# Optimization experiments

Measured on AMD Instinct MI355X. Metric: run time of the kernel, lower is better.

## Reference

```python
import jax, jax.numpy as jnp
import numpy as np
from jax import lax

T, S = 2000, 100          # trees, nodes per tree
N = T * S                 # total nodes
F = 256                   # in_feats (sent_hidden_size)
H = 256                   # h_feats (prop_hidden_size)


def _build_forest():
    # Random recursive forest: node j in each tree attaches to a uniform earlier node.
    rng = np.random.default_rng(0)
    pl = np.zeros((T, S), np.int64)    # local parent index
    dep = np.zeros((T, S), np.int64)
    rows = np.arange(T)
    for j in range(1, S):
        p = rng.integers(0, j, size=T)
        pl[:, j] = p
        dep[:, j] = dep[rows, p] + 1
    depth = dep.ravel()
    parent = (np.arange(T)[:, None] * S + pl).ravel()
    is_root = (np.arange(N) % S) == 0
    kids = np.arange(N)[~is_root]
    par = parent[~is_root]
    order = np.argsort(par, kind='stable')
    kids_s, par_s = kids[order], par[order]
    counts = np.bincount(par_s, minlength=N)
    C = int(counts.max())
    offsets = np.concatenate([[0], np.cumsum(counts)])
    pos = np.arange(len(kids_s)) - offsets[par_s]
    ch_all = np.full((N, C), N + 1, np.int32)   # pad with dummy zero-hidden row N+1
    ch_all[par_s, pos] = kids_s
    maxd = int(depth.max())
    L = maxd  # processed layers: depths 0..maxd-1 (deepest leaves stay zero, as in torch)
    layer_lists = [np.where(depth == d)[0] for d in range(L)]
    M = max(len(l) for l in layer_lists)
    layer_nodes = np.full((L, M), N, np.int32)  # pad writes to scratch row N
    child_idx = np.full((L, M, C), N + 1, np.int32)
    child_cnt = np.zeros((L, M), np.int32)
    for d, nd in enumerate(layer_lists):
        m = len(nd)
        layer_nodes[d, :m] = nd
        child_idx[d, :m] = ch_all[nd]
        child_cnt[d, :m] = counts[nd]
    root_idx = (np.arange(T) * S).astype(np.int32)
    return layer_nodes, child_idx, child_cnt, root_idx


def setup_inputs() -> dict:
    layer_nodes, child_idx, child_cnt, root_idx = _build_forest()
    key = jax.random.key(0)
    k1, k2, k3, k4, k5 = jax.random.split(key, 5)
    bound = 1.0 / np.sqrt(H)  # torch GRUCell default init
    u = lambda kk, sh: jax.random.uniform(kk, sh, jnp.float32, -bound, bound)
    return {
        'inputs': jax.random.normal(k1, (N, F), jnp.float32),
        'w_ih': u(k2, (3 * H, F)),
        'w_hh': u(k3, (3 * H, H)),
        'b_ih': u(k4, (3 * H,)),
        'b_hh': u(k5, (3 * H,)),
        'layer_nodes': jnp.asarray(layer_nodes),
        'child_idx': jnp.asarray(child_idx),
        'child_cnt': jnp.asarray(child_cnt),
        'root_idx': jnp.asarray(root_idx),
    }


def _gru(x, h, w_ih, w_hh, b_ih, b_hh):
    gi = x @ w_ih.T + b_ih
    gh = h @ w_hh.T + b_hh
    ir, iz, ig = jnp.split(gi, 3, axis=-1)
    hr, hz, hg = jnp.split(gh, 3, axis=-1)
    r = jax.nn.sigmoid(ir + hr)
    z = jax.nn.sigmoid(iz + hz)
    n = jnp.tanh(ig + r * hg)
    return (1.0 - z) * n + z * h


def _forward(inputs, w_ih, w_hh, b_ih, b_hh, layer_nodes, child_idx, child_cnt, root_idx):
    # rows N (scatter scratch for padded slots) and N+1 (always-zero child pad) appended
    x_all = jnp.concatenate([inputs, jnp.zeros((2, F), inputs.dtype)], axis=0)
    h0 = jnp.zeros((N + 2, H), inputs.dtype)

    def step(all_h, layer):
        nodes, cidx, ccnt = layer
        ch = all_h[cidx]                                        # [M, C, H]
        denom = jnp.maximum(ccnt, 1).astype(all_h.dtype)[:, None]
        h_prev = ch.sum(axis=1) / denom                         # mean over children; 0 for leaves
        new_h = _gru(x_all[nodes], h_prev, w_ih, w_hh, b_ih, b_hh)
        return all_h.at[nodes].set(new_h), None

    # process deepest layer first (reversed(range(max_depth)) in the original)
    xs = (layer_nodes[::-1], child_idx[::-1], child_cnt[::-1])
    all_h, _ = lax.scan(step, h0, xs)
    return all_h[root_idx]                                      # [T, H]


def reference(inputs, w_ih, w_hh, b_ih, b_hh, layer_nodes, child_idx, child_cnt, root_idx):
    return _forward(inputs, w_ih, w_hh, b_ih, b_hh, layer_nodes, child_idx, child_cnt, root_idx)
```

## Files before the change

kernel.cpp:

```cpp
#include <hip/hip_runtime.h>
#include <hip/hip_bf16.h>
#include <math.h>

#define N_NODES 200000
#define T_TREES 2000
#define S_NODES 100
#define F_DIM 256
#define H_DIM 256
#define G_DIM 768
#define D_MAX 28

typedef __attribute__((ext_vector_type(8))) short short8b;
typedef __attribute__((ext_vector_type(4))) float f32x4;

static __device__ __forceinline__ unsigned short f2bf(float x) {
    union { __hip_bfloat16 h; unsigned short u; } cv;
    cv.h = __float2bfloat16(x);
    return cv.u;
}
static __device__ __forceinline__ float bf2f(unsigned short u) {
    return __uint_as_float(((unsigned)u) << 16);
}
static __device__ __forceinline__ float fsig(float x) {
    return __builtin_amdgcn_rcpf(1.0f + __expf(-x));
}
static __device__ __forceinline__ float ftanh(float x) {
    return 1.0f - 2.0f * __builtin_amdgcn_rcpf(__expf(2.0f * x) + 1.0f);
}

__global__ void k_zero(float4* __restrict__ p, int n4) {
    float4 z = make_float4(0.f, 0.f, 0.f, 0.f);
    for (int i = blockIdx.x * blockDim.x + threadIdx.x; i < n4;
         i += gridDim.x * blockDim.x)
        p[i] = z;
}

__global__ void k_convx(const float* __restrict__ x, unsigned short* __restrict__ xb,
                        int n8) {
    for (int i = blockIdx.x * blockDim.x + threadIdx.x; i < n8;
         i += gridDim.x * blockDim.x) {
        const float4* px = (const float4*)(x + (size_t)i * 8);
        float4 u = px[0], v = px[1];
        short8b t;
        t[0] = f2bf(u.x); t[1] = f2bf(u.y); t[2] = f2bf(u.z); t[3] = f2bf(u.w);
        t[4] = f2bf(v.x); t[5] = f2bf(v.y); t[6] = f2bf(v.z); t[7] = f2bf(v.w);
        *(short8b*)(xb + (size_t)i * 8) = t;
    }
}

__global__ void k_findM(const int* __restrict__ ln, int LM, int* __restrict__ Mdev) {
    int local = 0x7F7F7F7F;
    for (int p = T_TREES + blockIdx.x * blockDim.x + threadIdx.x; p < LM;
         p += gridDim.x * blockDim.x)
        if (ln[p] < N_NODES && p < local) local = p;
#pragma unroll
    for (int off = 32; off; off >>= 1) {
        int o = __shfl_down(local, off);
        if (o < local) local = o;
    }
    __shared__ int wmin[4];
    if ((threadIdx.x & 63) == 0) wmin[threadIdx.x >> 6] = local;
    __syncthreads();
    if (threadIdx.x == 0) {
        int m = wmin[0];
        for (int i = 1; i < 4; ++i) if (wmin[i] < m) m = wmin[i];
        if (m < 0x7F7F7F7F) atomicMin(Mdev, m);
    }
}

__global__ void k_hist(const int* __restrict__ ln, const int* __restrict__ Mdev,
                       int* __restrict__ layer_cnt, int LM) {
    __shared__ int h[D_MAX];
    if (threadIdx.x < D_MAX) h[threadIdx.x] = 0;
    __syncthreads();
    const int M = Mdev[0];
    for (int p = blockIdx.x * blockDim.x + threadIdx.x; p < LM;
         p += gridDim.x * blockDim.x)
        if (ln[p] < N_NODES) {
            int d = p / M;
            if (d < D_MAX) atomicAdd(&h[d], 1);
        }
    __syncthreads();
    if (threadIdx.x < D_MAX && h[threadIdx.x])
        atomicAdd(&layer_cnt[threadIdx.x], h[threadIdx.x]);
}

__global__ void k_convw(const float* __restrict__ wi, const float* __restrict__ wh,
                        unsigned short* __restrict__ wib, unsigned short* __restrict__ whb) {
    int i = blockIdx.x * blockDim.x + threadIdx.x;
    if (i < G_DIM * F_DIM) {
        wib[i] = f2bf(wi[i]);
        whb[i] = f2bf(wh[i]);
    }
}

__global__ __launch_bounds__(256) void k_gemm_x(
    const unsigned short* __restrict__ xb,
    const unsigned short* __restrict__ wib,
    const float* __restrict__ b_ih,
    unsigned short* __restrict__ gi_all) {
    __shared__ unsigned short Bs[2][64][256];

    const int tid = threadIdx.x;
    const int wv = tid >> 6, lane = tid & 63;
    const int lr = lane & 15, kg = lane >> 4;
    const long m0 = (long)blockIdx.x * 128 + wv * 32;

    short8b A[2][8];
#pragma unroll
    for (int ms = 0; ms < 2; ++ms) {
        long r = m0 + ms * 16 + lr;
        if (r > N_NODES - 1) r = N_NODES - 1;
        const unsigned short* xp = xb + r * F_DIM + kg * 8;
#pragma unroll
        for (int ks = 0; ks < 8; ++ks)
            A[ms][ks] = *(const short8b*)(xp + ks * 32);
    }

    const int sr = tid >> 2, sp = tid & 3;
    const int psr = (sr >> 3) & 1;
    const int gp_off = (lr >> 2) * 8 + (lr & 3);
    const int prow = (gp_off >> 3) & 1;

    short8b st[8];
    {
        const unsigned short* src = wib + (size_t)sr * F_DIM;
#pragma unroll
        for (int q = 0; q < 4; ++q) {
            int c = sp * 16 + q * 64;
            st[2 * q]     = *(const short8b*)(src + c);
            st[2 * q + 1] = *(const short8b*)(src + c + 8);
        }
#pragma unroll
        for (int q = 0; q < 4; ++q) {
            int slot = (sp >> 1) + 2 * q;
            int pc = ((slot ^ psr) << 5) + (sp & 1) * 16;
            *(short8b*)&Bs[0][sr][pc]     = st[2 * q];
            *(short8b*)&Bs[0][sr][pc + 8] = st[2 * q + 1];
        }
    }
    __syncthreads();

    const f32x4 zf = {0.f, 0.f, 0.f, 0.f};

    for (int nt = 0; nt < 12; ++nt) {
        const int cur = nt & 1;
        if (nt < 11) {
            const unsigned short* src = wib + (size_t)((nt + 1) * 64 + sr) * F_DIM;
#pragma unroll
            for (int q = 0; q < 4; ++q) {
                int c = sp * 16 + q * 64;
                st[2 * q]     = *(const short8b*)(src + c);
                st[2 * q + 1] = *(const short8b*)(src + c + 8);
            }
        }
#pragma unroll
        for (int nsp = 0; nsp < 2; ++nsp) {
            f32x4 aP0 = zf, aQ0 = zf, aP1 = zf, aQ1 = zf;
            const int rP = nsp * 32 + gp_off;
#pragma unroll
            for (int ks = 0; ks < 8; ++ks) {
                const int pc = ((ks ^ prow) << 5) + kg * 8;
                short8b BP = *(const short8b*)&Bs[cur][rP][pc];
                short8b BQ = *(const short8b*)&Bs[cur][rP + 4][pc];
                aP0 = __builtin_amdgcn_mfma_f32_16x16x32_bf16(BP, A[0][ks], aP0, 0, 0, 0);
                aQ0 = __builtin_amdgcn_mfma_f32_16x16x32_bf16(BQ, A[0][ks], aQ0, 0, 0, 0);
                aP1 = __builtin_amdgcn_mfma_f32_16x16x32_bf16(BP, A[1][ks], aP1, 0, 0, 0);
                aQ1 = __builtin_amdgcn_mfma_f32_16x16x32_bf16(BQ, A[1][ks], aQ1, 0, 0, 0);
            }
            const int g0 = nt * 64 + nsp * 32 + kg * 8;
            f32x4 b0 = *(const f32x4*)(b_ih + g0);
            f32x4 b1 = *(const f32x4*)(b_ih + g0 + 4);
            long m = m0 + lr;
            if (m < N_NODES) {
                short8b pk;
#pragma unroll
                for (int i = 0; i < 4; ++i) {
                    pk[i]     = f2bf(aP0[i] + b0[i]);
                    pk[4 + i] = f2bf(aQ0[i] + b1[i]);
                }
                *(short8b*)(gi_all + m * G_DIM + g0) = pk;
            }
            m = m0 + 16 + lr;
            if (m < N_NODES) {
                short8b pk;
#pragma unroll
                for (int i = 0; i < 4; ++i) {
                    pk[i]     = f2bf(aP1[i] + b0[i]);
                    pk[4 + i] = f2bf(aQ1[i] + b1[i]);
                }
                *(short8b*)(gi_all + m * G_DIM + g0) = pk;
            }
        }
        if (nt < 11) {
            __syncthreads();
#pragma unroll
            for (int q = 0; q < 4; ++q) {
                int slot = (sp >> 1) + 2 * q;
                int pc = ((slot ^ psr) << 5) + (sp & 1) * 16;
                *(short8b*)&Bs[cur ^ 1][sr][pc]     = st[2 * q];
                *(short8b*)&Bs[cur ^ 1][sr][pc + 8] = st[2 * q + 1];
            }
            __syncthreads();
        }
    }
}

#define LOADC2(buf, ns_, kh_)                                                  \
  _Pragma("unroll")                                                            \
  for (int kk = 0; kk < 4; ++kk)                                               \
    buf[kk] = *(const short8b*)(whb +                                          \
        (size_t)(512 + cb + (ns_) * 16 + lr) * H_DIM + ((kh_) * 4 + kk) * 32 + kg * 8);

#define MMACP(c_)                                                              \
  _Pragma("unroll")                                                            \
  for (int ks = 0; ks < 8; ++ks) {                                             \
    const int cch = ks * 4 + kg;                                               \
    const int pc = ((cch & 24) | ((cch ^ lr) & 7)) << 3;                       \
    short8b A0 = *(const short8b*)&Ab[lr][pc];                                 \
    short8b A1 = *(const short8b*)&Ab[16 + lr][pc];                            \
    _Pragma("unroll")                                                          \
    for (int ns = 0; ns < 2; ++ns) {                                           \
      acc[c_][0][ns] = __builtin_amdgcn_mfma_f32_16x16x32_bf16(                \
          A0, Bp[c_][ns][ks], acc[c_][0][ns], 0, 0, 0);                        \
      acc[c_][1][ns] = __builtin_amdgcn_mfma_f32_16x16x32_bf16(                \
          A1, Bp[c_][ns][ks], acc[c_][1][ns], 0, 0, 0);                        \
    }                                                                          \
  }

#define MMAC2(buf, ns_, kh_)                                                   \
  _Pragma("unroll")                                                            \
  for (int kk = 0; kk < 4; ++kk) {                                             \
    const int ks = (kh_) * 4 + kk;                                             \
    const int cch = ks * 4 + kg;                                               \
    const int pc = ((cch & 24) | ((cch ^ lr) & 7)) << 3;                       \
    short8b A0 = *(const short8b*)&Ab[lr][pc];                                 \
    short8b A1 = *(const short8b*)&Ab[16 + lr][pc];                            \
    acc[2][0][ns_] = __builtin_amdgcn_mfma_f32_16x16x32_bf16(                  \
        A0, buf[kk], acc[2][0][ns_], 0, 0, 0);                                 \
    acc[2][1][ns_] = __builtin_amdgcn_mfma_f32_16x16x32_bf16(                  \
        A1, buf[kk], acc[2][1][ns_], 0, 0, 0);                                 \
  }

__global__ __launch_bounds__(512, 2) void k_layer(
    const int* __restrict__ layer_nodes,
    const int* __restrict__ child_idx,
    const int* __restrict__ child_cnt,
    const int* __restrict__ Mdev,
    const int* __restrict__ layer_cnt,
    const unsigned short* __restrict__ whb,
    const unsigned short* __restrict__ gi_all,
    const float* __restrict__ b_hh,
    unsigned short* __restrict__ h_all,
    float* __restrict__ out,
    int d, int C) {
    __shared__ unsigned short Ab[32][256];
    __shared__ unsigned short Ag[32][776];
    __shared__ int Nd[32];

    const int cntd = layer_cnt[d];
    if (cntd == 0) return;
    const int M = Mdev[0];
    const int ntiles = (cntd + 31) >> 5;
    if (blockIdx.x >= ntiles) return;
    const long pbase = (long)d * M;

    const int tid = threadIdx.x;
    const int wv = tid >> 6, lane = tid & 63;
    const int lr = lane & 15, kg = lane >> 4;
    const int cb = wv * 32;

    short8b Bp[2][2][8];
#pragma unroll
    for (int c = 0; c < 2; ++c)
#pragma unroll
        for (int ns = 0; ns < 2; ++ns) {
            const unsigned short* bp =
                whb + (size_t)(c * 256 + cb + ns * 16 + lr) * H_DIM + kg * 8;
#pragma unroll
            for (int ks = 0; ks < 8; ++ks)
                Bp[c][ns][ks] = *(const short8b*)(bp + ks * 32);
        }

    float bh[3][2];
#pragma unroll
    for (int c = 0; c < 3; ++c)
#pragma unroll
        for (int ns = 0; ns < 2; ++ns)
            bh[c][ns] = b_hh[c * 256 + cb + ns * 16 + lr];

    const int srow = tid >> 4;
    const int sc = tid & 15;

    for (int tile = blockIdx.x; tile < ntiles; tile += gridDim.x) {
        __syncthreads();
        {
            int idx = tile * 32 + srow;
            int node = (idx < cntd) ? layer_nodes[pbase + idx] : -1;
            if (sc == 0) Nd[srow] = node;
            {
                const unsigned short* gp =
                    gi_all + (size_t)(node >= 0 ? node : 0) * G_DIM;
#pragma unroll
                for (int pass = 0; pass < 6; ++pass) {
                    int col = sc * 8 + pass * 128;
                    *(short8b*)&Ag[srow][col] = *(const short8b*)(gp + col);
                }
            }
            int cc = 0;
            const int* ch = nullptr;
            if (node >= 0) {
                cc = child_cnt[pbase + idx];
                ch = child_idx + (size_t)(pbase + idx) * C;
            }
            float inv = 1.0f / (float)(cc > 0 ? cc : 1);
            float sum[16];
#pragma unroll
            for (int i = 0; i < 16; ++i) sum[i] = 0.f;
            for (int c = 0; c < cc; ++c) {
                int kid = ch[c];
                const unsigned short* hr = h_all + (size_t)kid * H_DIM + sc * 16;
                short8b v0 = *(const short8b*)hr;
                short8b v1 = *(const short8b*)(hr + 8);
#pragma unroll
                for (int i = 0; i < 8; ++i) {
                    sum[i]     += bf2f((unsigned short)v0[i]);
                    sum[8 + i] += bf2f((unsigned short)v1[i]);
                }
            }
            short8b q0, q1;
#pragma unroll
            for (int i = 0; i < 8; ++i) {
                q0[i] = f2bf(sum[i] * inv);
                q1[i] = f2bf(sum[8 + i] * inv);
            }
            const int g = srow & 7;
            const int c0 = 2 * sc, c1 = 2 * sc + 1;
            *(short8b*)&Ab[srow][((c0 & 24) | ((c0 ^ g) & 7)) << 3] = q0;
            *(short8b*)&Ab[srow][((c1 & 24) | ((c1 ^ g) & 7)) << 3] = q1;
        }
        __syncthreads();

        const f32x4 zf = {0.f, 0.f, 0.f, 0.f};
        f32x4 acc[3][2][2];
#pragma unroll
        for (int c = 0; c < 3; ++c)
#pragma unroll
            for (int ms = 0; ms < 2; ++ms)
#pragma unroll
                for (int ns = 0; ns < 2; ++ns) acc[c][ms][ns] = zf;

        short8b C2a[4], C2b[4];
        LOADC2(C2a, 0, 0);
        MMACP(0);
        LOADC2(C2b, 0, 1);
        MMAC2(C2a, 0, 0);
        LOADC2(C2a, 1, 0);
        MMACP(1);
        MMAC2(C2b, 0, 1);
        LOADC2(C2b, 1, 1);
        MMAC2(C2a, 1, 0);
        MMAC2(C2b, 1, 1);

#pragma unroll
        for (int ms = 0; ms < 2; ++ms)
#pragma unroll
            for (int i = 0; i < 4; ++i) {
                const int rl = ms * 16 + kg * 4 + i;
                const int nd = Nd[rl];
                if (nd < 0) continue;
#pragma unroll
                for (int ns = 0; ns < 2; ++ns) {
                    const int k = cb + ns * 16 + lr;
                    const int kc = k >> 3;
                    const int hp_off = (((kc & 24) | ((kc ^ rl) & 7)) << 3) + (k & 7);
                    float hp = bf2f(Ab[rl][hp_off]);
                    float xr = bf2f(Ag[rl][k])       + acc[0][ms][ns][i] + bh[0][ns];
                    float xz = bf2f(Ag[rl][256 + k]) + acc[1][ms][ns][i] + bh[1][ns];
                    float r = fsig(xr);
                    float z = fsig(xz);
                    float n = ftanh(bf2f(Ag[rl][512 + k]) +
                                    r * (acc[2][ms][ns][i] + bh[2][ns]));
                    float h = (1.0f - z) * n + z * hp;
                    if (d == 0) {
                        out[(size_t)(nd / S_NODES) * H_DIM + k] = h;
                    } else {
                        h_all[(size_t)nd * H_DIM + k] = f2bf(h);
                    }
                }
            }
    }
}

extern "C" void kernel_launch(void* const* d_in, const int* in_sizes, int n_in,
                              void* d_out, int out_size, void* d_ws, size_t ws_size,
                              hipStream_t stream) {
    const float* inputs = (const float*)d_in[0];
    const float* w_ih   = (const float*)d_in[1];
    const float* w_hh   = (const float*)d_in[2];
    const float* b_ih   = (const float*)d_in[3];
    const float* b_hh   = (const float*)d_in[4];
    const int* layer_nodes = (const int*)d_in[5];
    const int* child_idx   = (const int*)d_in[6];
    const int* child_cnt   = (const int*)d_in[7];

    const int LM = in_sizes[5];
    const int C  = in_sizes[6] / in_sizes[5];

    char* w = (char*)d_ws;
    size_t o = 0;
    auto alloc = [&](size_t bytes) {
        void* p = w + o;
        o += (bytes + 255) & ~(size_t)255;
        return p;
    };
    unsigned short* wib    = (unsigned short*)alloc((size_t)G_DIM * F_DIM * 2);
    unsigned short* whb    = (unsigned short*)alloc((size_t)G_DIM * H_DIM * 2);
    unsigned short* xb     = (unsigned short*)alloc((size_t)N_NODES * F_DIM * 2);
    unsigned short* h_all  = (unsigned short*)alloc((size_t)N_NODES * H_DIM * 2);
    unsigned short* gi_all = (unsigned short*)alloc((size_t)N_NODES * G_DIM * 2);
    int*            Mdev      = (int*)alloc(4);
    int*            layer_cnt = (int*)alloc(D_MAX * 4);
    (void)ws_size;

    hipMemsetAsync(Mdev, 0x7F, 4, stream);
    hipMemsetAsync(layer_cnt, 0, D_MAX * 4, stream);

    k_zero<<<2048, 256, 0, stream>>>((float4*)h_all, N_NODES * H_DIM * 2 / 16);
    k_convx<<<2048, 256, 0, stream>>>(inputs, xb, N_NODES * F_DIM / 8);
    k_findM<<<256, 256, 0, stream>>>(layer_nodes, LM, Mdev);
    k_hist<<<256, 256, 0, stream>>>(layer_nodes, Mdev, layer_cnt, LM);
    k_convw<<<(G_DIM * F_DIM + 255) / 256, 256, 0, stream>>>(w_ih, w_hh, wib, whb);

    k_gemm_x<<<(N_NODES + 127) / 128, 256, 0, stream>>>(xb, wib, b_ih, gi_all);

    for (int d = D_MAX - 1; d >= 0; --d)
        k_layer<<<512, 512, 0, stream>>>(layer_nodes, child_idx, child_cnt,
                                         Mdev, layer_cnt, whb, gi_all, b_hh,
                                         h_all, (float*)d_out, d, C);
}
```

Before: 1.041 ms.

## Parallelize child-hidden gather across lanes and reswizzle input-GEMM weight LDS layout

The child-mean gather in the per-layer GRU kernel is restructured so each wavefront handles two rows at a time, with four lane groups loading different children in parallel and reducing with cross-lane shuffles. Before, one thread walked all children of a node serially. The aim is more memory-level parallelism and shorter dependent load chains on the latency-bound gather. Separately, the weight tile in the input-projection GEMM uses a finer XOR swizzle to cut LDS bank conflicts on the MFMA operand reads. The cost is extra shuffle instructions and idle lanes when a node has fewer than four children.

Result: slower. 1.337 ms (+28.4%).

```diff
diff --git a/kernel.cpp b/kernel.cpp
--- a/kernel.cpp
+++ b/kernel.cpp
@@ -118,9 +118,9 @@
     }
 
     const int sr = tid >> 2, sp = tid & 3;
-    const int psr = (sr >> 3) & 1;
+    const int hs = (sr & 3) | (((sr >> 3) & 1) << 2);
     const int gp_off = (lr >> 2) * 8 + (lr & 3);
-    const int prow = (gp_off >> 3) & 1;
+    const int hq = (lr & 3) | (((lr >> 2) & 1) << 2);
 
     short8b st[8];
     {
@@ -133,10 +133,9 @@
         }
 #pragma unroll
         for (int q = 0; q < 4; ++q) {
-            int slot = (sp >> 1) + 2 * q;
-            int pc = ((slot ^ psr) << 5) + (sp & 1) * 16;
-            *(short8b*)&Bs[0][sr][pc]     = st[2 * q];
-            *(short8b*)&Bs[0][sr][pc + 8] = st[2 * q + 1];
+            int c0 = sp * 2 + q * 8, c1 = c0 + 1;
+            *(short8b*)&Bs[0][sr][((c0 & 24) | ((c0 ^ hs) & 7)) << 3] = st[2 * q];
+            *(short8b*)&Bs[0][sr][((c1 & 24) | ((c1 ^ hs) & 7)) << 3] = st[2 * q + 1];
         }
     }
     __syncthreads();
@@ -160,7 +159,8 @@
             const int rP = nsp * 32 + gp_off;
 #pragma unroll
             for (int ks = 0; ks < 8; ++ks) {
-                const int pc = ((ks ^ prow) << 5) + kg * 8;
+                const int c = ks * 4 + kg;
+                const int pc = ((c & 24) | ((c ^ hq) & 7)) << 3;
                 short8b BP = *(const short8b*)&Bs[cur][rP][pc];
                 short8b BQ = *(const short8b*)&Bs[cur][rP + 4][pc];
                 aP0 = __builtin_amdgcn_mfma_f32_16x16x32_bf16(BP, A[0][ks], aP0, 0, 0, 0);
@@ -196,10 +196,9 @@
             __syncthreads();
 #pragma unroll
             for (int q = 0; q < 4; ++q) {
-                int slot = (sp >> 1) + 2 * q;
-                int pc = ((slot ^ psr) << 5) + (sp & 1) * 16;
-                *(short8b*)&Bs[cur ^ 1][sr][pc]     = st[2 * q];
-                *(short8b*)&Bs[cur ^ 1][sr][pc + 8] = st[2 * q + 1];
+                int c0 = sp * 2 + q * 8, c1 = c0 + 1;
+                *(short8b*)&Bs[cur ^ 1][sr][((c0 & 24) | ((c0 ^ hs) & 7)) << 3] = st[2 * q];
+                *(short8b*)&Bs[cur ^ 1][sr][((c1 & 24) | ((c1 ^ hs) & 7)) << 3] = st[2 * q + 1];
             }
             __syncthreads();
         }
@@ -291,53 +290,94 @@
 
     const int srow = tid >> 4;
     const int sc = tid & 15;
+    const int cl = lane >> 4;
+    const int chk = lane & 15;
 
     for (int tile = blockIdx.x; tile < ntiles; tile += gridDim.x) {
         __syncthreads();
         {
             int idx = tile * 32 + srow;
-            int node = (idx < cntd) ? layer_nodes[pbase + idx] : -1;
-            if (sc == 0) Nd[srow] = node;
-            {
-                const unsigned short* gp =
-                    gi_all + (size_t)(node >= 0 ? node : 0) * G_DIM;
-#pragma unroll
-                for (int pass = 0; pass < 6; ++pass) {
-                    int col = sc * 8 + pass * 128;
-                    *(short8b*)&Ag[srow][col] = *(const short8b*)(gp + col);
-                }
-            }
-            int cc = 0;
-            const int* ch = nullptr;
-            if (node >= 0) {
-                cc = child_cnt[pbase + idx];
-                ch = child_idx + (size_t)(pbase + idx) * C;
-            }
-            float inv = 1.0f / (float)(cc > 0 ? cc : 1);
-            float sum[16];
-#pragma unroll
-            for (int i = 0; i < 16; ++i) sum[i] = 0.f;
-            for (int c = 0; c < cc; ++c) {
-                int kid = ch[c];
-                const unsigned short* hr = h_all + (size_t)kid * H_DIM + sc * 16;
-                short8b v0 = *(const short8b*)hr;
-                short8b v1 = *(const short8b*)(hr + 8);
-#pragma unroll
-                for (int i = 0; i < 8; ++i) {
-                    sum[i]     += bf2f((unsigned short)v0[i]);
-                    sum[8 + i] += bf2f((unsigned short)v1[i]);
-                }
-            }
-            short8b q0, q1;
-#pragma unroll
-            for (int i = 0; i < 8; ++i) {
-                q0[i] = f2bf(sum[i] * inv);
-                q1[i] = f2bf(sum[8 + i] * inv);
-            }
-            const int g = srow & 7;
-            const int c0 = 2 * sc, c1 = 2 * sc + 1;
-            *(short8b*)&Ab[srow][((c0 & 24) | ((c0 ^ g) & 7)) << 3] = q0;
-            *(short8b*)&Ab[srow][((c1 & 24) | ((c1 ^ g) & 7)) << 3] = q1;
+            int node = (idx < cntd) ? layer_nodes[pbase + idx] : 0;
+            const unsigned short* gp = gi_all + (size_t)node * G_DIM;
+#pragma unroll
+            for (int pass = 0; pass < 6; ++pass) {
+                int col = sc * 8 + pass * 128;
+                *(short8b*)&Ag[srow][col] = *(const short8b*)(gp + col);
+            }
+        }
+#pragma unroll
+        for (int pp = 0; pp < 2; ++pp) {
+            const int r0 = wv * 4 + pp * 2;
+            int nodes2[2], ccs[2];
+            const int* chp[2];
+            float sum[2][16];
+            short8b va[2][2];
+            bool act[2];
+#pragma unroll
+            for (int rr = 0; rr < 2; ++rr) {
+                int idx = tile * 32 + r0 + rr;
+                int node = (idx < cntd) ? layer_nodes[pbase + idx] : -1;
+                nodes2[rr] = node;
+                int cc = 0; const int* ch = nullptr;
+                if (node >= 0) {
+                    cc = child_cnt[pbase + idx];
+                    ch = child_idx + (size_t)(pbase + idx) * C;
+                }
+                ccs[rr] = cc; chp[rr] = ch;
+#pragma unroll
+                for (int i = 0; i < 16; ++i) sum[rr][i] = 0.f;
+                act[rr] = (cl < cc);
+                if (act[rr]) {
+                    const unsigned short* hr =
+                        h_all + (size_t)ch[cl] * H_DIM + chk * 16;
+                    va[rr][0] = *(const short8b*)hr;
+                    va[rr][1] = *(const short8b*)(hr + 8);
+                }
+            }
+#pragma unroll
+            for (int rr = 0; rr < 2; ++rr) {
+                if (act[rr]) {
+#pragma unroll
+                    for (int i = 0; i < 8; ++i) {
+                        sum[rr][i]     += bf2f((unsigned short)va[rr][0][i]);
+                        sum[rr][8 + i] += bf2f((unsigned short)va[rr][1][i]);
+                    }
+                }
+                for (int b = 4; b < ccs[rr]; b += 4) {
+                    int c = b + cl;
+                    if (c < ccs[rr]) {
+                        const unsigned short* hr =
+                            h_all + (size_t)chp[rr][c] * H_DIM + chk * 16;
+                        short8b w0 = *(const short8b*)hr;
+                        short8b w1 = *(const short8b*)(hr + 8);
+#pragma unroll
+                        for (int i = 0; i < 8; ++i) {
+                            sum[rr][i]     += bf2f((unsigned short)w0[i]);
+                            sum[rr][8 + i] += bf2f((unsigned short)w1[i]);
+                        }
+                    }
+                }
+#pragma unroll
+                for (int i = 0; i < 16; ++i) {
+                    sum[rr][i] += __shfl_xor(sum[rr][i], 16);
+                    sum[rr][i] += __shfl_xor(sum[rr][i], 32);
+                }
+                if (cl == 0) {
+                    const int row = r0 + rr;
+                    float inv = 1.0f / (float)(ccs[rr] > 0 ? ccs[rr] : 1);
+                    short8b q0, q1;
+#pragma unroll
+                    for (int i = 0; i < 8; ++i) {
+                        q0[i] = f2bf(sum[rr][i] * inv);
+                        q1[i] = f2bf(sum[rr][8 + i] * inv);
+                    }
+                    const int g = row & 7;
+                    const int c0 = 2 * chk, c1 = c0 + 1;
+                    *(short8b*)&Ab[row][((c0 & 24) | ((c0 ^ g) & 7)) << 3] = q0;
+                    *(short8b*)&Ab[row][((c1 & 24) | ((c1 ^ g) & 7)) << 3] = q1;
+                    if (chk == 0) Nd[row] = nodes2[rr];
+                }
+            }
         }
         __syncthreads();
 
```

## Split child-mean gather into separate kernel and reswizzle x-GEMM shared layout

Applied to the files above, without the earlier changes.

Moves the per-layer child hidden-state averaging out of the fused GRU layer kernel into a dedicated gather kernel that writes a compact hprev buffer, which the layer kernel then reads directly. The aim is more parallelism and latency hiding for the irregular child gathers, instead of stalling the MFMA kernel. In exchange it adds a kernel launch per layer and an extra write and read of hprev through memory. The x-projection GEMM's shared-memory B tile uses a new XOR swizzle to reduce bank conflicts, and D_MAX drops from 28 to 24, removing layer launches that are assumed to be empty.

Result: slower. 1.083 ms (+4.0%).

```diff
diff --git a/kernel.cpp b/kernel.cpp
--- a/kernel.cpp
+++ b/kernel.cpp
@@ -8,7 +8,7 @@
 #define F_DIM 256
 #define H_DIM 256
 #define G_DIM 768
-#define D_MAX 28
+#define D_MAX 24
 
 typedef __attribute__((ext_vector_type(8))) short short8b;
 typedef __attribute__((ext_vector_type(4))) float f32x4;
@@ -118,9 +118,9 @@
     }
 
     const int sr = tid >> 2, sp = tid & 3;
-    const int psr = (sr >> 3) & 1;
+    const int hs = (sr & 3) | (((sr >> 3) & 1) << 2);
     const int gp_off = (lr >> 2) * 8 + (lr & 3);
-    const int prow = (gp_off >> 3) & 1;
+    const int hq = (lr & 3) | (((lr >> 2) & 1) << 2);
 
     short8b st[8];
     {
@@ -133,10 +133,9 @@
         }
 #pragma unroll
         for (int q = 0; q < 4; ++q) {
-            int slot = (sp >> 1) + 2 * q;
-            int pc = ((slot ^ psr) << 5) + (sp & 1) * 16;
-            *(short8b*)&Bs[0][sr][pc]     = st[2 * q];
-            *(short8b*)&Bs[0][sr][pc + 8] = st[2 * q + 1];
+            int c0 = sp * 2 + q * 8, c1 = c0 + 1;
+            *(short8b*)&Bs[0][sr][((c0 & 24) | ((c0 ^ hs) & 7)) << 3] = st[2 * q];
+            *(short8b*)&Bs[0][sr][((c1 & 24) | ((c1 ^ hs) & 7)) << 3] = st[2 * q + 1];
         }
     }
     __syncthreads();
@@ -160,7 +159,8 @@
             const int rP = nsp * 32 + gp_off;
 #pragma unroll
             for (int ks = 0; ks < 8; ++ks) {
-                const int pc = ((ks ^ prow) << 5) + kg * 8;
+                const int c = ks * 4 + kg;
+                const int pc = ((c & 24) | ((c ^ hq) & 7)) << 3;
                 short8b BP = *(const short8b*)&Bs[cur][rP][pc];
                 short8b BQ = *(const short8b*)&Bs[cur][rP + 4][pc];
                 aP0 = __builtin_amdgcn_mfma_f32_16x16x32_bf16(BP, A[0][ks], aP0, 0, 0, 0);
@@ -196,12 +196,57 @@
             __syncthreads();
 #pragma unroll
             for (int q = 0; q < 4; ++q) {
-                int slot = (sp >> 1) + 2 * q;
-                int pc = ((slot ^ psr) << 5) + (sp & 1) * 16;
-                *(short8b*)&Bs[cur ^ 1][sr][pc]     = st[2 * q];
-                *(short8b*)&Bs[cur ^ 1][sr][pc + 8] = st[2 * q + 1];
+                int c0 = sp * 2 + q * 8, c1 = c0 + 1;
+                *(short8b*)&Bs[cur ^ 1][sr][((c0 & 24) | ((c0 ^ hs) & 7)) << 3] = st[2 * q];
+                *(short8b*)&Bs[cur ^ 1][sr][((c1 & 24) | ((c1 ^ hs) & 7)) << 3] = st[2 * q + 1];
             }
             __syncthreads();
+        }
+    }
+}
+
+__global__ void k_gather(
+    const int* __restrict__ layer_nodes,
+    const int* __restrict__ child_idx,
+    const int* __restrict__ child_cnt,
+    const int* __restrict__ Mdev,
+    const int* __restrict__ layer_cnt,
+    const unsigned short* __restrict__ h_all,
+    unsigned short* __restrict__ hprev,
+    int d, int C) {
+    const int cntd = layer_cnt[d];
+    if (cntd == 0) return;
+    const int M = Mdev[0];
+    const long pbase = (long)d * M;
+    const int total = cntd * 8;
+
+    for (int t = blockIdx.x * blockDim.x + threadIdx.x; t < total;
+         t += gridDim.x * blockDim.x) {
+        const int idx = t >> 3;
+        const int cb = (t & 7) * 32;
+        const int cc = child_cnt[pbase + idx];
+        const int* ch = child_idx + (size_t)(pbase + idx) * C;
+        float sum[32];
+#pragma unroll
+        for (int i = 0; i < 32; ++i) sum[i] = 0.f;
+        for (int c = 0; c < cc; ++c) {
+            const unsigned short* hr = h_all + (size_t)ch[c] * H_DIM + cb;
+#pragma unroll
+            for (int q = 0; q < 4; ++q) {
+                short8b v = *(const short8b*)(hr + q * 8);
+#pragma unroll
+                for (int j = 0; j < 8; ++j)
+                    sum[q * 8 + j] += bf2f((unsigned short)v[j]);
+            }
+        }
+        const float inv = 1.0f / (float)(cc > 0 ? cc : 1);
+        unsigned short* dst = hprev + (size_t)idx * H_DIM + cb;
+#pragma unroll
+        for (int q = 0; q < 4; ++q) {
+            short8b pk;
+#pragma unroll
+            for (int j = 0; j < 8; ++j) pk[j] = f2bf(sum[q * 8 + j] * inv);
+            *(short8b*)(dst + q * 8) = pk;
         }
     }
 }
@@ -244,16 +289,15 @@
 
 __global__ __launch_bounds__(512, 2) void k_layer(
     const int* __restrict__ layer_nodes,
-    const int* __restrict__ child_idx,
-    const int* __restrict__ child_cnt,
     const int* __restrict__ Mdev,
     const int* __restrict__ layer_cnt,
     const unsigned short* __restrict__ whb,
+    const unsigned short* __restrict__ hprev,
     const unsigned short* __restrict__ gi_all,
     const float* __restrict__ b_hh,
     unsigned short* __restrict__ h_all,
     float* __restrict__ out,
-    int d, int C) {
+    int d) {
     __shared__ unsigned short Ab[32][256];
     __shared__ unsigned short Ag[32][776];
     __shared__ int Nd[32];
@@ -307,33 +351,10 @@
                     *(short8b*)&Ag[srow][col] = *(const short8b*)(gp + col);
                 }
             }
-            int cc = 0;
-            const int* ch = nullptr;
-            if (node >= 0) {
-                cc = child_cnt[pbase + idx];
-                ch = child_idx + (size_t)(pbase + idx) * C;
-            }
-            float inv = 1.0f / (float)(cc > 0 ? cc : 1);
-            float sum[16];
-#pragma unroll
-            for (int i = 0; i < 16; ++i) sum[i] = 0.f;
-            for (int c = 0; c < cc; ++c) {
-                int kid = ch[c];
-                const unsigned short* hr = h_all + (size_t)kid * H_DIM + sc * 16;
-                short8b v0 = *(const short8b*)hr;
-                short8b v1 = *(const short8b*)(hr + 8);
-#pragma unroll
-                for (int i = 0; i < 8; ++i) {
-                    sum[i]     += bf2f((unsigned short)v0[i]);
-                    sum[8 + i] += bf2f((unsigned short)v1[i]);
-                }
-            }
-            short8b q0, q1;
-#pragma unroll
-            for (int i = 0; i < 8; ++i) {
-                q0[i] = f2bf(sum[i] * inv);
-                q1[i] = f2bf(sum[8 + i] * inv);
-            }
+            const unsigned short* hp =
+                hprev + (size_t)(idx < cntd ? idx : 0) * H_DIM + sc * 16;
+            short8b q0 = *(const short8b*)hp;
+            short8b q1 = *(const short8b*)(hp + 8);
             const int g = srow & 7;
             const int c0 = 2 * sc, c1 = 2 * sc + 1;
             *(short8b*)&Ab[srow][((c0 & 24) | ((c0 ^ g) & 7)) << 3] = q0;
@@ -418,6 +439,7 @@
     unsigned short* whb    = (unsigned short*)alloc((size_t)G_DIM * H_DIM * 2);
     unsigned short* xb     = (unsigned short*)alloc((size_t)N_NODES * F_DIM * 2);
     unsigned short* h_all  = (unsigned short*)alloc((size_t)N_NODES * H_DIM * 2);
+    unsigned short* hprev  = (unsigned short*)alloc((size_t)N_NODES * H_DIM * 2);
     unsigned short* gi_all = (unsigned short*)alloc((size_t)N_NODES * G_DIM * 2);
     int*            Mdev      = (int*)alloc(4);
     int*            layer_cnt = (int*)alloc(D_MAX * 4);
@@ -434,8 +456,11 @@
 
     k_gemm_x<<<(N_NODES + 127) / 128, 256, 0, stream>>>(xb, wib, b_ih, gi_all);
 
-    for (int d = D_MAX - 1; d >= 0; --d)
-        k_layer<<<512, 512, 0, stream>>>(layer_nodes, child_idx, child_cnt,
-                                         Mdev, layer_cnt, whb, gi_all, b_hh,
-                                         h_all, (float*)d_out, d, C);
-}
+    for (int d = D_MAX - 1; d >= 0; --d) {
+        k_gather<<<1024, 256, 0, stream>>>(layer_nodes, child_idx, child_cnt,
+                                           Mdev, layer_cnt, h_all, hprev, d, C);
+        k_layer<<<512, 512, 0, stream>>>(layer_nodes, Mdev, layer_cnt,
+                                         whb, hprev, gi_all, b_hh,
+                                         h_all, (float*)d_out, d);
+    }
+}
```
